# Kernel tuning notes

Measured on AMD Instinct MI355X. Metric: run time of the kernel, lower is better.

## Reference

```python
import jax, jax.numpy as jnp
import numpy as np

# static config (Phi-3-like with GQA)
B, S, H, HKV, D, BS = 2, 2048, 32, 8, 128, 64
HID = H * D
NB = B * (S // BS)  # total cache blocks
THETA = 10000.0


def rotate_half(x):
    x1, x2 = jnp.split(x, 2, axis=-1)
    return jnp.concatenate([-x2, x1], axis=-1)


def rope_cos_sin(positions):
    # positions: [T] int -> cos/sin [T, D]
    inv_freq = 1.0 / (THETA ** (jnp.arange(0, D, 2, dtype=jnp.float32) / D))
    freqs = positions.astype(jnp.float32)[:, None] * inv_freq[None, :]
    emb = jnp.concatenate([freqs, freqs], axis=-1)
    return jnp.cos(emb), jnp.sin(emb)


def setup_inputs() -> dict:
    key = jax.random.key(0)
    k1, k2, k3 = jax.random.split(key, 3)
    T = B * S
    hidden_states = jax.random.normal(k1, (T, HID), dtype=jnp.float32)
    w_qkv = jax.random.normal(k2, ((H + 2 * HKV) * D, HID), dtype=jnp.float32) * 0.02
    w_o = jax.random.normal(k3, (HID, H * D), dtype=jnp.float32) * 0.02
    k_cache = jnp.zeros((NB, BS, HKV, D), dtype=jnp.float32)
    v_cache = jnp.zeros((NB, BS, HKV, D), dtype=jnp.float32)
    position_ids = jnp.tile(jnp.arange(S, dtype=jnp.int32), B)  # per-token positions (prefill)
    block_offsets = jnp.arange(NB, dtype=jnp.int32).reshape(B, S // BS)
    return dict(hidden_states=hidden_states, w_qkv=w_qkv, w_o=w_o,
                k_cache=k_cache, v_cache=v_cache, position_ids=position_ids,
                block_offsets=block_offsets, window_size=1024)


def reference(hidden_states, w_qkv, w_o, k_cache, v_cache, position_ids, block_offsets, window_size):
    # fused qkv projection + split
    qkv = hidden_states @ w_qkv.T  # [T, (H+2*HKV)*D]
    q, k, v = jnp.split(qkv, [H * D, H * D + HKV * D], axis=-1)
    q = q.reshape(-1, H, D)
    k = k.reshape(-1, HKV, D)
    v = v.reshape(-1, HKV, D)

    # rotary embedding on flattened tokens
    cos, sin = rope_cos_sin(position_ids)  # [T, D]
    cos, sin = cos[:, None, :], sin[:, None, :]
    q = q * cos + rotate_half(q) * sin
    k = k * cos + rotate_half(k) * sin

    # fill paged KV cache: token t of seq b -> block block_offsets[b, t//BS], slot t%BS
    flat_blocks = block_offsets.reshape(-1)  # [NB]
    k_blk = k.reshape(NB, BS, HKV, D)
    v_blk = v.reshape(NB, BS, HKV, D)
    k_cache = k_cache.at[flat_blocks].set(k_blk)
    v_cache = v_cache.at[flat_blocks].set(v_blk)

    # paged attention: gather per-sequence K/V through the block table
    k_seq = k_cache[block_offsets].reshape(B, S, HKV, D)
    v_seq = v_cache[block_offsets].reshape(B, S, HKV, D)

    G = H // HKV  # query heads per kv head (GQA)
    qh = q.reshape(B, S, HKV, G, D)
    scale = 1.0 / jnp.sqrt(jnp.float32(D))
    scores = jnp.einsum('bshgd,bthd->bhgst', qh, k_seq) * scale  # [B,HKV,G,S,S]

    # causal + sliding-window mask: j <= i and i - j < window_size
    i = jnp.arange(S)[:, None]
    j = jnp.arange(S)[None, :]
    mask = (j <= i) & ((i - j) < window_size)  # [S,S]
    scores = jnp.where(mask[None, None, None], scores, jnp.finfo(scores.dtype).min)
    probs = jax.nn.softmax(scores, axis=-1)

    out = jnp.einsum('bhgst,bthd->bshgd', probs, v_seq)  # [B,S,HKV,G,D]
    out = out.reshape(B * S, H * D)
    return out @ w_o.T  # [T, HID]
```

## Files before the change

kernel.cpp:

```cpp
#include <hip/hip_runtime.h>
#include <hip/hip_bf16.h>
#include <stdint.h>

typedef unsigned short u16;
typedef __attribute__((ext_vector_type(8))) short short8;
typedef __attribute__((ext_vector_type(8))) unsigned short u16x8;
typedef __attribute__((ext_vector_type(4))) float f32x4;
typedef __attribute__((ext_vector_type(16))) float f32x16;

#define B_    2
#define S_    2048
#define H_    32
#define HKV_  8
#define D_    128
#define HID_  4096
#define QKVW_ 6144

__device__ __forceinline__ u16 f2bf(float f){
  uint32_t b = __builtin_bit_cast(uint32_t, f);
  b += 0x7FFFu + ((b >> 16) & 1u);
  return (u16)(b >> 16);
}
__device__ __forceinline__ float bf2f(u16 h){
  uint32_t b = ((uint32_t)h) << 16;
  return __builtin_bit_cast(float, b);
}
__device__ __forceinline__ u16 bfc(float f){
  __hip_bfloat16 h = __float2bfloat16(f);
  return __builtin_bit_cast(u16, h);
}
__device__ __forceinline__ uint32_t cvtpk(float a, float b){
  uint32_t r;
  asm("v_cvt_pk_bf16_f32 %0, %1, %2" : "=v"(r) : "v"(a), "v"(b));
  return r;
}
__device__ __forceinline__ void pl32swap(uint32_t &a, uint32_t &b){
  asm volatile("v_permlane32_swap_b32 %0, %1" : "+v"(a), "+v"(b));
}

__device__ __forceinline__ void gload16(const u16* g, u16* l){
  __builtin_amdgcn_global_load_lds((const __attribute__((address_space(1))) void*)g,
                                   (__attribute__((address_space(3))) void*)l, 16, 0, 0);
}

__global__ void cvt_kernel(const float* __restrict__ src, u16* __restrict__ dst, int n4){
  int i = blockIdx.x * blockDim.x + threadIdx.x;
  int stride = gridDim.x * blockDim.x;
  for (; i < n4; i += stride){
    float4 v = reinterpret_cast<const float4*>(src)[i];
    union { u16 u[4]; unsigned long long ll; } o;
    o.u[0] = f2bf(v.x); o.u[1] = f2bf(v.y); o.u[2] = f2bf(v.z); o.u[3] = f2bf(v.w);
    reinterpret_cast<unsigned long long*>(dst)[i] = o.ll;
  }
}

__global__ void rope_table_kernel(float2* __restrict__ tab){
  int idx = blockIdx.x * blockDim.x + threadIdx.x;
  if (idx >= S_ * 64) return;
  int pos = idx >> 6, p = idx & 63;
  float inv = powf(10000.0f, -(float)p / 64.0f);
  float ang = (float)pos * inv;
  tab[idx] = make_float2(cosf(ang), sinf(ang));
}

__global__ void rope_k_kernel(u16* __restrict__ qkv, const int* __restrict__ pos_ids,
                              const float2* __restrict__ tab){
  int t = blockIdx.x;
  int pos = pos_ids[t];
  const float2* tb = tab + pos * 64;
  u16* row = qkv + (size_t)t * QKVW_ + HID_;
  for (int it = threadIdx.x; it < HKV_ * 64; it += 256){
    int hh = it >> 6, p = it & 63;
    int base = hh * D_;
    float x1 = bf2f(row[base + p]);
    float x2 = bf2f(row[base + 64 + p]);
    float2 cs = tb[p];
    row[base + p]      = f2bf(x1 * cs.x - x2 * cs.y);
    row[base + 64 + p] = f2bf(x2 * cs.x + x1 * cs.y);
  }
}

#define MFMA_(a, b, c)   __builtin_amdgcn_mfma_f32_16x16x32_bf16((a), (b), (c), 0, 0, 0)
#define MFMA32_(a, b, c) __builtin_amdgcn_mfma_f32_32x32x16_bf16((a), (b), (c), 0, 0, 0)

__global__ __launch_bounds__(256) void gemm128(const u16* __restrict__ A, const u16* __restrict__ B,
                                               u16* __restrict__ C, int M, int N, int K){
  __shared__ u16 As[128*64];
  __shared__ u16 Bs[128*64];
  const int tid  = threadIdx.x;
  const int wave = tid >> 6, lane = tid & 63;
  const int hi = lane >> 4, lo = lane & 15;
  const int bn = blockIdx.x, bm = blockIdx.y;
  const int wm = (wave >> 1) * 64, wn = (wave & 1) * 64;
  f32x4 acc[4][4] = {};

  const u16* ap[4]; const u16* bp[4];
  u16* lA[4]; u16* lB[4];
  #pragma unroll
  for (int p = 0; p < 4; p++){
    int e   = p*2048 + wave*512 + lane*8;
    int row = e >> 6;
    int cs  = ((e >> 3) & 7) ^ (row & 7);
    ap[p] = A + (size_t)(bm*128 + row) * K + cs*8;
    bp[p] = B + (size_t)(bn*128 + row) * K + cs*8;
    lA[p] = &As[p*2048 + wave*512];
    lB[p] = &Bs[p*2048 + wave*512];
  }
  const int sw = lo & 7;
  const int nk = K >> 6;
  for (int t = 0; t < nk; t++){
    #pragma unroll
    for (int p = 0; p < 4; p++){
      gload16(ap[p], lA[p]);
      gload16(bp[p], lB[p]);
      ap[p] += 64; bp[p] += 64;
    }
    __syncthreads();
    #pragma unroll
    for (int kk = 0; kk < 2; kk++){
      short8 af[4], bf[4];
      int sz = ((kk*4 + hi) ^ sw) * 8;
      #pragma unroll
      for (int mt = 0; mt < 4; mt++) af[mt] = *(const short8*)&As[(wm + mt*16 + lo)*64 + sz];
      #pragma unroll
      for (int nt = 0; nt < 4; nt++) bf[nt] = *(const short8*)&Bs[(wn + nt*16 + lo)*64 + sz];
      #pragma unroll
      for (int mt = 0; mt < 4; mt++)
        #pragma unroll
        for (int nt = 0; nt < 4; nt++)
          acc[mt][nt] = MFMA_(af[mt], bf[nt], acc[mt][nt]);
    }
    __syncthreads();
  }
  #pragma unroll
  for (int mt = 0; mt < 4; mt++){
    int row = bm*128 + wm + mt*16 + 4*hi;
    #pragma unroll
    for (int nt = 0; nt < 4; nt++){
      int col = bn*128 + wn + nt*16 + lo;
      #pragma unroll
      for (int r = 0; r < 4; r++)
        C[(size_t)(row + r)*N + col] = f2bf(acc[mt][nt][r]);
    }
  }
}

__global__ __launch_bounds__(512, 2) void gemm256(const u16* __restrict__ A, const u16* __restrict__ B,
                                                  float* __restrict__ C, int M, int N, int K, int nbn){
  __shared__ u16 As[2][16384];
  __shared__ u16 Bs[2][16384];
  const int tid = threadIdx.x;
  const int wave = tid >> 6, lane = tid & 63, lo = lane & 15, hi = lane >> 4;
  const int wr = wave >> 2, wc = wave & 3;
  const int sw = lo & 7;

  const int nwg = gridDim.x, bid = blockIdx.x, cpx = nwg >> 3;
  const int wg = (bid & 7) * cpx + (bid >> 3);
  const int bm = wg / nbn, bn = wg - bm * nbn;

  f32x4 acc[8][4] = {};

  const int pr0 = tid >> 3;
  const int sc0 = (tid & 7) ^ (pr0 & 7);
  const u16* aS0 = A + ((size_t)(bm*256 + pr0      ))*K + sc0*8;
  const u16* aS1 = A + ((size_t)(bm*256 + pr0 + 128))*K + sc0*8;
  const u16* aS2 = A + ((size_t)(bm*256 + pr0 + 64 ))*K + sc0*8;
  const u16* aS3 = A + ((size_t)(bm*256 + pr0 + 192))*K + sc0*8;
  const u16* bS0 = B + ((size_t)(bn*256 + pr0      ))*K + sc0*8;
  const u16* bS1 = B + ((size_t)(bn*256 + pr0 + 64 ))*K + sc0*8;
  const u16* bS2 = B + ((size_t)(bn*256 + pr0 + 128))*K + sc0*8;
  const u16* bS3 = B + ((size_t)(bn*256 + pr0 + 192))*K + sc0*8;
  const int dOfs = tid * 8;

  gload16(bS0, &Bs[0][dOfs]);        gload16(bS1, &Bs[0][4096 + dOfs]);
  gload16(bS2, &Bs[0][8192 + dOfs]); gload16(bS3, &Bs[0][12288 + dOfs]);
  gload16(aS0, &As[0][dOfs]);        gload16(aS1, &As[0][4096 + dOfs]);
  gload16(aS2, &As[0][8192 + dOfs]); gload16(aS3, &As[0][12288 + dOfs]);
  asm volatile("s_waitcnt vmcnt(0)" ::: "memory");
  __builtin_amdgcn_s_barrier();

  const int nk = K >> 6;
  for (int t = 0; t < nk; ++t){
    const int cur = t & 1, nxt = cur ^ 1;
    const u16* Ac = &As[cur][0];
    const u16* Bc = &Bs[cur][0];
    u16* An = &As[nxt][0];
    u16* Bn = &Bs[nxt][0];
    const size_t ko = (size_t)(t + 1) * 64;
    const bool more = (t + 1 < nk);
    short8 avr[4], bvr[8];

    #define RD_A(q) \
      _Pragma("unroll") for (int mt = 0; mt < 2; mt++) \
        _Pragma("unroll") for (int kk = 0; kk < 2; kk++){ \
          int ra = wr*128 + (q)*32 + mt*16 + lo; \
          int fo = ((ra & 63) << 6) + ((ra & 64) ? 8192 : 0) + ((ra & 128) ? 4096 : 0) \
                 + ((((kk << 2) + hi) ^ sw) << 3); \
          avr[mt*2 + kk] = *(const short8*)&Ac[fo]; \
        }
    #define DO_MFMA(q) \
      __builtin_amdgcn_s_setprio(1); \
      _Pragma("unroll") for (int mt = 0; mt < 2; mt++) \
        _Pragma("unroll") for (int nt = 0; nt < 4; nt++) \
          _Pragma("unroll") for (int kk = 0; kk < 2; kk++) \
            acc[(q)*2 + mt][nt] = MFMA_(avr[mt*2 + kk], bvr[nt*2 + kk], acc[(q)*2 + mt][nt]); \
      __builtin_amdgcn_s_setprio(0);

    #pragma unroll
    for (int nt = 0; nt < 4; nt++)
      #pragma unroll
      for (int kk = 0; kk < 2; kk++){
        int rb = wc*64 + nt*16 + lo;
        int fo = (rb << 6) + ((((kk << 2) + hi) ^ sw) << 3);
        bvr[nt*2 + kk] = *(const short8*)&Bc[fo];
      }
    RD_A(0)
    if (more){ gload16(bS0 + ko, Bn + dOfs); gload16(bS1 + ko, Bn + 4096 + dOfs); }
    __builtin_amdgcn_s_barrier();
    DO_MFMA(0)
    __builtin_amdgcn_s_barrier();

    RD_A(1)
    if (more){
      gload16(bS2 + ko, Bn + 8192 + dOfs); gload16(bS3 + ko, Bn + 12288 + dOfs);
      asm volatile("s_waitcnt vmcnt(4)" ::: "memory");
    } else {
      asm volatile("s_waitcnt vmcnt(0)" ::: "memory");
    }
    __builtin_amdgcn_sched_barrier(0);
    __builtin_amdgcn_s_barrier();
    DO_MFMA(1)
    __builtin_amdgcn_s_barrier();

    RD_A(2)
    if (more){ gload16(aS0 + ko, An + dOfs); gload16(aS1 + ko, An + 4096 + dOfs); }
    __builtin_amdgcn_s_barrier();
    DO_MFMA(2)
    __builtin_amdgcn_s_barrier();

    RD_A(3)
    if (more){ gload16(aS2 + ko, An + 8192 + dOfs); gload16(aS3 + ko, An + 12288 + dOfs); }
    asm volatile("s_waitcnt vmcnt(2)" ::: "memory");
    __builtin_amdgcn_sched_barrier(0);
    __builtin_amdgcn_s_barrier();
    DO_MFMA(3)
    __builtin_amdgcn_s_barrier();
    #undef RD_A
    #undef DO_MFMA
  }

  #pragma unroll
  for (int mtg = 0; mtg < 8; mtg++){
    int row = bm*256 + wr*128 + mtg*16 + 4*hi;
    #pragma unroll
    for (int nt = 0; nt < 4; nt++){
      int col = bn*256 + wc*64 + nt*16 + lo;
      #pragma unroll
      for (int r = 0; r < 4; r++)
        C[(size_t)(row + r)*N + col] = acc[mtg][nt][r];
    }
  }
}

__global__ __launch_bounds__(256, 2) void attn_kernel(const u16* __restrict__ qkv, u16* __restrict__ out,
                                                      const int* __restrict__ winp,
                                                      const int* __restrict__ pos_ids,
                                                      const float2* __restrict__ tab){
  const int id = blockIdx.x;
  const int hkv = id & 7;
  const int qtr = (id >> 3) & 15;
  const int gb  = id >> 7;
  const int qt  = (qtr + 3*gb) & 15;
  const int g = gb & 3, b = gb >> 2;
  const int h = hkv*4 + g;
  const int q0 = qt * 128;
  const int tid = threadIdx.x, wave = tid >> 6, lane = tid & 63;
  const int ql = lane & 31, hl = lane >> 5;
  const int win = winp[0];

  __shared__ u16 Ks[2][64*128];
  __shared__ u16 VT[2][128*64];

  const int qw = q0 + wave*32;
  short8 qf[8];
  {
    const u16* qp = qkv + (size_t)(b*S_ + qw + ql)*QKVW_ + h*D_ + hl*8;
    #pragma unroll
    for (int c = 0; c < 8; c++) qf[c] = *(const short8*)(qp + c*16);
    const float QS = 0.08838834764831845f * 1.4426950408889634f;
    int pos = pos_ids[b*S_ + qw + ql];
    const float2* tb = tab + pos*64 + hl*8;
    #pragma unroll
    for (int c = 0; c < 4; c++)
      #pragma unroll
      for (int i = 0; i < 8; i++){
        float2 cs = tb[c*16 + i];
        float x1 = bf2f((u16)qf[c][i]), x2 = bf2f((u16)qf[c+4][i]);
        qf[c][i]   = (short)bfc((x1*cs.x - x2*cs.y) * QS);
        qf[c+4][i] = (short)bfc((x2*cs.x + x1*cs.y) * QS);
      }
  }

  f32x16 acc[4] = {};
  float m_r = -3.0e38f, l_r = 0.0f;

  int js = q0 - (win - 1); if (js < 0) js = 0; js &= ~63;
  const int nt = (q0 + 128 - js) >> 6;

  const u16* Kg = qkv + (size_t)HID_ + hkv*D_;
  const u16* Vg = qkv + (size_t)HID_ + HKV_*D_ + hkv*D_;
  const int jp = tid & 31, d0 = (tid >> 5) * 16;

  const u16* ksrc[4];
  #pragma unroll
  for (int p = 0; p < 4; p++){
    int e = p*256 + tid;
    int row = e >> 4;
    int ss = (e & 15) ^ (row & 15);
    ksrc[p] = Kg + (size_t)(b*S_ + js + row)*QKVW_ + ss*8;
  }
  const u16* vsrc = Vg + (size_t)(b*S_ + js + 2*jp)*QKVW_ + d0;

  u16x8 vr0, vr1, vr2, vr3;
  {
    #pragma unroll
    for (int p = 0; p < 4; p++) gload16(ksrc[p], &Ks[0][p*2048 + wave*512]);
    vr0 = *(const u16x8*)(vsrc);
    vr1 = *(const u16x8*)(vsrc + 8);
    vr2 = *(const u16x8*)(vsrc + QKVW_);
    vr3 = *(const u16x8*)(vsrc + QKVW_ + 8);
    uint32_t* VT32 = (uint32_t*)&VT[0][0];
    #pragma unroll
    for (int i = 0; i < 8; i++){
      int da = d0 + i, db = d0 + 8 + i;
      VT32[da*32 + (jp ^ ((da & 7) << 2))] = (uint32_t)vr0[i] | ((uint32_t)vr2[i] << 16);
      VT32[db*32 + (jp ^ ((db & 7) << 2))] = (uint32_t)vr1[i] | ((uint32_t)vr3[i] << 16);
    }
  }
  __syncthreads();

  for (int t = 0; t < nt; t++){
    const int jc = js + t*64;
    const int cur = t & 1, nxt = cur ^ 1;
    const bool more = (t + 1 < nt);
    if (more){
      const size_t adv = (size_t)(t+1) * 64 * QKVW_;
      #pragma unroll
      for (int p = 0; p < 4; p++) gload16(ksrc[p] + adv, &Ks[nxt][p*2048 + wave*512]);
      const u16* vp = vsrc + adv;
      vr0 = *(const u16x8*)(vp);
      vr1 = *(const u16x8*)(vp + 8);
      vr2 = *(const u16x8*)(vp + QKVW_);
      vr3 = *(const u16x8*)(vp + QKVW_ + 8);
    }
    if (jc <= qw + 31 && jc + 63 >= qw - win + 1){
      f32x16 s0 = {}, s1 = {};
      const int sl = ql & 15;
      __builtin_amdgcn_s_setprio(1);
      #pragma unroll
      for (int c = 0; c < 8; c++){
        int so = (((c*2 + hl) ^ sl) * 8);
        short8 k0 = *(const short8*)&Ks[cur][ql*128 + so];
        short8 k1 = *(const short8*)&Ks[cur][(32 + ql)*128 + so];
        s0 = MFMA32_(k0, qf[c], s0);
        s1 = MFMA32_(k1, qf[c], s1);
      }
      __builtin_amdgcn_s_setprio(0);
      const int qa = qw + ql;
      const bool fullv = (jc + 63 <= qw) && (jc >= qw + 32 - win);
      if (!fullv){
        #pragma unroll
        for (int r = 0; r < 16; r++){
          int j0 = jc + (r&3) + 8*(r>>2) + 4*hl;
          if (j0 > qa || qa - j0 >= win) s0[r] = -3.0e38f;
          int j1 = j0 + 32;
          if (j1 > qa || qa - j1 >= win) s1[r] = -3.0e38f;
        }
      }
      float mx = s0[0];
      #pragma unroll
      for (int r = 1; r < 16; r++) mx = fmaxf(mx, s0[r]);
      #pragma unroll
      for (int r = 0; r < 16; r++) mx = fmaxf(mx, s1[r]);
      mx = fmaxf(mx, __shfl_xor(mx, 32));
      if (__any(mx > m_r + 8.0f)){
        float mn = fmaxf(m_r, mx);
        float al = exp2f(m_r - mn);
        m_r = mn; l_r *= al;
        #pragma unroll
        for (int r = 0; r < 16; r++){
          float a = __shfl(al, (r&3) + 8*(r>>2) + 4*hl);
          acc[0][r] *= a; acc[1][r] *= a; acc[2][r] *= a; acc[3][r] *= a;
        }
      }
      float ps = 0.f;
      if (fullv){
        #pragma unroll
        for (int r = 0; r < 16; r++){
          s0[r] = exp2f(s0[r] - m_r); s1[r] = exp2f(s1[r] - m_r);
          ps += s0[r] + s1[r];
        }
      } else {
        #pragma unroll
        for (int r = 0; r < 16; r++){
          s0[r] = s0[r] > -1e37f ? exp2f(s0[r] - m_r) : 0.f;
          s1[r] = s1[r] > -1e37f ? exp2f(s1[r] - m_r) : 0.f;
          ps += s0[r] + s1[r];
        }
      }
      ps += __shfl_xor(ps, 32);
      l_r += ps;
      short8 pa[4];
      #define MKFRAG(dst, P, o) { \
        uint32_t x1 = cvtpk(P[o+0], P[o+1]), x2 = cvtpk(P[o+2], P[o+3]); \
        uint32_t y1 = cvtpk(P[o+4], P[o+5]), y2 = cvtpk(P[o+6], P[o+7]); \
        pl32swap(x1, y1); pl32swap(x2, y2); \
        union { uint32_t w[4]; short8 v; } u_; \
        u_.w[0] = x1; u_.w[1] = x2; u_.w[2] = y1; u_.w[3] = y2; \
        dst = u_.v; }
      MKFRAG(pa[0], s0, 0)
      MKFRAG(pa[1], s0, 8)
      MKFRAG(pa[2], s1, 0)
      MKFRAG(pa[3], s1, 8)
      #undef MKFRAG
      __builtin_amdgcn_s_setprio(1);
      #pragma unroll
      for (int dt = 0; dt < 4; dt++){
        const int dr = dt*32 + ql;
        const u16* vb = &VT[cur][dr*64];
        const int sb = dr & 7;
        #pragma unroll
        for (int ks = 0; ks < 4; ks++){
          short8 vf = *(const short8*)&vb[(((ks*2 + hl) ^ sb) * 8)];
          acc[dt] = MFMA32_(pa[ks], vf, acc[dt]);
        }
      }
      __builtin_amdgcn_s_setprio(0);
    }
    if (more){
      uint32_t* VT32 = (uint32_t*)&VT[nxt][0];
      #pragma unroll
      for (int i = 0; i < 8; i++){
        int da = d0 + i, db = d0 + 8 + i;
        VT32[da*32 + (jp ^ ((da & 7) << 2))] = (uint32_t)vr0[i] | ((uint32_t)vr2[i] << 16);
        VT32[db*32 + (jp ^ ((db & 7) << 2))] = (uint32_t)vr1[i] | ((uint32_t)vr3[i] << 16);
      }
      __syncthreads();
    }
  }
  #pragma unroll
  for (int r = 0; r < 16; r++){
    int qrow = (r&3) + 8*(r>>2) + 4*hl;
    float lr = __shfl(l_r, qrow);
    float invl = 1.0f / lr;
    size_t ro = (size_t)(b*S_ + qw + qrow)*HID_ + h*D_ + ql;
    out[ro     ] = f2bf(acc[0][r] * invl);
    out[ro + 32] = f2bf(acc[1][r] * invl);
    out[ro + 64] = f2bf(acc[2][r] * invl);
    out[ro + 96] = f2bf(acc[3][r] * invl);
  }
}

extern "C" void kernel_launch(void* const* d_in, const int* in_sizes, int n_in,
                              void* d_out, int out_size, void* d_ws, size_t ws_size,
                              hipStream_t stream) {
  const float* hs   = (const float*)d_in[0];
  const float* wqkv = (const float*)d_in[1];
  const float* wo   = (const float*)d_in[2];
  const int* pos  = (const int*)d_in[5];
  const int* winp = (const int*)d_in[7];
  float* out = (float*)d_out;

  u16* hsb = (u16*)d_ws;
  u16* wqb = hsb + (size_t)HID_*HID_;
  u16* wob = wqb + (size_t)QKVW_*HID_;
  u16* qkv = wob + (size_t)HID_*HID_;
  u16* att = qkv + (size_t)(B_*S_)*QKVW_;
  float2* tab = (float2*)(att + (size_t)(B_*S_)*HID_);

  cvt_kernel<<<2048, 256, 0, stream>>>(hs,   hsb, HID_*HID_/4);
  cvt_kernel<<<2048, 256, 0, stream>>>(wqkv, wqb, QKVW_*HID_/4);
  cvt_kernel<<<2048, 256, 0, stream>>>(wo,   wob, HID_*HID_/4);
  rope_table_kernel<<<(S_*64 + 255)/256, 256, 0, stream>>>(tab);
  gemm128<<<dim3(QKVW_/128, (B_*S_)/128), 256, 0, stream>>>(hsb, wqb, qkv, B_*S_, QKVW_, HID_);
  rope_k_kernel<<<B_*S_, 256, 0, stream>>>(qkv, pos, tab);
  attn_kernel<<<1024, 256, 0, stream>>>(qkv, att, winp, pos, tab);
  gemm256<<<(B_*S_/256)*(HID_/256), 512, 0, stream>>>(att, wob, out, B_*S_, HID_, HID_, HID_/256);
}
```

Baseline: 524.7 us.

## Replace QKV projection GEMM with templated 256x192 double-buffered pipelined GEMM

```diff
diff --git a/kernel.cpp b/kernel.cpp
--- a/kernel.cpp
+++ b/kernel.cpp
@@ -83,72 +83,13 @@
 #define MFMA_(a, b, c)   __builtin_amdgcn_mfma_f32_16x16x32_bf16((a), (b), (c), 0, 0, 0)
 #define MFMA32_(a, b, c) __builtin_amdgcn_mfma_f32_32x32x16_bf16((a), (b), (c), 0, 0, 0)
 
-__global__ __launch_bounds__(256) void gemm128(const u16* __restrict__ A, const u16* __restrict__ B,
-                                               u16* __restrict__ C, int M, int N, int K){
-  __shared__ u16 As[128*64];
-  __shared__ u16 Bs[128*64];
-  const int tid  = threadIdx.x;
-  const int wave = tid >> 6, lane = tid & 63;
-  const int hi = lane >> 4, lo = lane & 15;
-  const int bn = blockIdx.x, bm = blockIdx.y;
-  const int wm = (wave >> 1) * 64, wn = (wave & 1) * 64;
-  f32x4 acc[4][4] = {};
-
-  const u16* ap[4]; const u16* bp[4];
-  u16* lA[4]; u16* lB[4];
-  #pragma unroll
-  for (int p = 0; p < 4; p++){
-    int e   = p*2048 + wave*512 + lane*8;
-    int row = e >> 6;
-    int cs  = ((e >> 3) & 7) ^ (row & 7);
-    ap[p] = A + (size_t)(bm*128 + row) * K + cs*8;
-    bp[p] = B + (size_t)(bn*128 + row) * K + cs*8;
-    lA[p] = &As[p*2048 + wave*512];
-    lB[p] = &Bs[p*2048 + wave*512];
-  }
-  const int sw = lo & 7;
-  const int nk = K >> 6;
-  for (int t = 0; t < nk; t++){
-    #pragma unroll
-    for (int p = 0; p < 4; p++){
-      gload16(ap[p], lA[p]);
-      gload16(bp[p], lB[p]);
-      ap[p] += 64; bp[p] += 64;
-    }
-    __syncthreads();
-    #pragma unroll
-    for (int kk = 0; kk < 2; kk++){
-      short8 af[4], bf[4];
-      int sz = ((kk*4 + hi) ^ sw) * 8;
-      #pragma unroll
-      for (int mt = 0; mt < 4; mt++) af[mt] = *(const short8*)&As[(wm + mt*16 + lo)*64 + sz];
-      #pragma unroll
-      for (int nt = 0; nt < 4; nt++) bf[nt] = *(const short8*)&Bs[(wn + nt*16 + lo)*64 + sz];
-      #pragma unroll
-      for (int mt = 0; mt < 4; mt++)
-        #pragma unroll
-        for (int nt = 0; nt < 4; nt++)
-          acc[mt][nt] = MFMA_(af[mt], bf[nt], acc[mt][nt]);
-    }
-    __syncthreads();
-  }
-  #pragma unroll
-  for (int mt = 0; mt < 4; mt++){
-    int row = bm*128 + wm + mt*16 + 4*hi;
-    #pragma unroll
-    for (int nt = 0; nt < 4; nt++){
-      int col = bn*128 + wn + nt*16 + lo;
-      #pragma unroll
-      for (int r = 0; r < 4; r++)
-        C[(size_t)(row + r)*N + col] = f2bf(acc[mt][nt][r]);
-    }
-  }
-}
-
-__global__ __launch_bounds__(512, 2) void gemm256(const u16* __restrict__ A, const u16* __restrict__ B,
-                                                  float* __restrict__ C, int M, int N, int K, int nbn){
+template<int BN, int CF>
+__global__ __launch_bounds__(512, 2) void gemmN(const u16* __restrict__ A, const u16* __restrict__ B,
+                                                void* __restrict__ Cv, int M, int N, int K, int nbn){
+  constexpr int NBP = BN / 64;
+  constexpr int WN  = BN / 4;
   __shared__ u16 As[2][16384];
-  __shared__ u16 Bs[2][16384];
+  __shared__ u16 Bs[2][BN*64];
   const int tid = threadIdx.x;
   const int wave = tid >> 6, lane = tid & 63, lo = lane & 15, hi = lane >> 4;
   const int wr = wave >> 2, wc = wave & 3;
@@ -158,7 +99,7 @@
   const int wg = (bid & 7) * cpx + (bid >> 3);
   const int bm = wg / nbn, bn = wg - bm * nbn;
 
-  f32x4 acc[8][4] = {};
+  f32x4 acc[8][NBP] = {};
 
   const int pr0 = tid >> 3;
   const int sc0 = (tid & 7) ^ (pr0 & 7);
@@ -166,14 +107,14 @@
   const u16* aS1 = A + ((size_t)(bm*256 + pr0 + 128))*K + sc0*8;
   const u16* aS2 = A + ((size_t)(bm*256 + pr0 + 64 ))*K + sc0*8;
   const u16* aS3 = A + ((size_t)(bm*256 + pr0 + 192))*K + sc0*8;
-  const u16* bS0 = B + ((size_t)(bn*256 + pr0      ))*K + sc0*8;
-  const u16* bS1 = B + ((size_t)(bn*256 + pr0 + 64 ))*K + sc0*8;
-  const u16* bS2 = B + ((size_t)(bn*256 + pr0 + 128))*K + sc0*8;
-  const u16* bS3 = B + ((size_t)(bn*256 + pr0 + 192))*K + sc0*8;
+  const u16* bS[NBP];
+  #pragma unroll
+  for (int p = 0; p < NBP; p++)
+    bS[p] = B + ((size_t)(bn*BN + pr0 + p*64))*K + sc0*8;
   const int dOfs = tid * 8;
 
-  gload16(bS0, &Bs[0][dOfs]);        gload16(bS1, &Bs[0][4096 + dOfs]);
-  gload16(bS2, &Bs[0][8192 + dOfs]); gload16(bS3, &Bs[0][12288 + dOfs]);
+  #pragma unroll
+  for (int p = 0; p < NBP; p++) gload16(bS[p], &Bs[0][p*4096 + dOfs]);
   gload16(aS0, &As[0][dOfs]);        gload16(aS1, &As[0][4096 + dOfs]);
   gload16(aS2, &As[0][8192 + dOfs]); gload16(aS3, &As[0][12288 + dOfs]);
   asm volatile("s_waitcnt vmcnt(0)" ::: "memory");
@@ -188,7 +129,7 @@
     u16* Bn = &Bs[nxt][0];
     const size_t ko = (size_t)(t + 1) * 64;
     const bool more = (t + 1 < nk);
-    short8 avr[4], bvr[8];
+    short8 avr[4], bvr[2*NBP];
 
     #define RD_A(q) \
       _Pragma("unroll") for (int mt = 0; mt < 2; mt++) \
@@ -201,28 +142,32 @@
     #define DO_MFMA(q) \
       __builtin_amdgcn_s_setprio(1); \
       _Pragma("unroll") for (int mt = 0; mt < 2; mt++) \
-        _Pragma("unroll") for (int nt = 0; nt < 4; nt++) \
+        _Pragma("unroll") for (int nt = 0; nt < NBP; nt++) \
           _Pragma("unroll") for (int kk = 0; kk < 2; kk++) \
             acc[(q)*2 + mt][nt] = MFMA_(avr[mt*2 + kk], bvr[nt*2 + kk], acc[(q)*2 + mt][nt]); \
       __builtin_amdgcn_s_setprio(0);
 
     #pragma unroll
-    for (int nt = 0; nt < 4; nt++)
+    for (int nt = 0; nt < NBP; nt++)
       #pragma unroll
       for (int kk = 0; kk < 2; kk++){
-        int rb = wc*64 + nt*16 + lo;
+        int rb = wc*WN + nt*16 + lo;
         int fo = (rb << 6) + ((((kk << 2) + hi) ^ sw) << 3);
         bvr[nt*2 + kk] = *(const short8*)&Bc[fo];
       }
     RD_A(0)
-    if (more){ gload16(bS0 + ko, Bn + dOfs); gload16(bS1 + ko, Bn + 4096 + dOfs); }
+    if (more){ gload16(bS[0] + ko, Bn + dOfs); gload16(bS[1] + ko, Bn + 4096 + dOfs); }
     __builtin_amdgcn_s_barrier();
     DO_MFMA(0)
     __builtin_amdgcn_s_barrier();
 
     RD_A(1)
     if (more){
-      gload16(bS2 + ko, Bn + 8192 + dOfs); gload16(bS3 + ko, Bn + 12288 + dOfs);
+      if constexpr (NBP == 4){
+        gload16(bS[2] + ko, Bn + 8192 + dOfs); gload16(bS[3] + ko, Bn + 12288 + dOfs);
+      } else {
+        gload16(bS[2] + ko, Bn + 8192 + dOfs); gload16(aS0 + ko, An + dOfs);
+      }
       asm volatile("s_waitcnt vmcnt(4)" ::: "memory");
     } else {
       asm volatile("s_waitcnt vmcnt(0)" ::: "memory");
@@ -233,13 +178,25 @@
     __builtin_amdgcn_s_barrier();
 
     RD_A(2)
-    if (more){ gload16(aS0 + ko, An + dOfs); gload16(aS1 + ko, An + 4096 + dOfs); }
+    if (more){
+      if constexpr (NBP == 4){
+        gload16(aS0 + ko, An + dOfs); gload16(aS1 + ko, An + 4096 + dOfs);
+      } else {
+        gload16(aS1 + ko, An + 4096 + dOfs); gload16(aS2 + ko, An + 8192 + dOfs);
+      }
+    }
     __builtin_amdgcn_s_barrier();
     DO_MFMA(2)
     __builtin_amdgcn_s_barrier();
 
     RD_A(3)
-    if (more){ gload16(aS2 + ko, An + 8192 + dOfs); gload16(aS3 + ko, An + 12288 + dOfs); }
+    if (more){
+      if constexpr (NBP == 4){
+        gload16(aS2 + ko, An + 8192 + dOfs); gload16(aS3 + ko, An + 12288 + dOfs);
+      } else {
+        gload16(aS3 + ko, An + 12288 + dOfs);
+      }
+    }
     asm volatile("s_waitcnt vmcnt(2)" ::: "memory");
     __builtin_amdgcn_sched_barrier(0);
     __builtin_amdgcn_s_barrier();
@@ -253,11 +210,13 @@
   for (int mtg = 0; mtg < 8; mtg++){
     int row = bm*256 + wr*128 + mtg*16 + 4*hi;
     #pragma unroll
-    for (int nt = 0; nt < 4; nt++){
-      int col = bn*256 + wc*64 + nt*16 + lo;
-      #pragma unroll
-      for (int r = 0; r < 4; r++)
-        C[(size_t)(row + r)*N + col] = acc[mtg][nt][r];
+    for (int nt = 0; nt < NBP; nt++){
+      int col = bn*BN + wc*WN + nt*16 + lo;
+      #pragma unroll
+      for (int r = 0; r < 4; r++){
+        if (CF == 0) ((u16*)Cv)[(size_t)(row + r)*N + col] = f2bf(acc[mtg][nt][r]);
+        else         ((float*)Cv)[(size_t)(row + r)*N + col] = acc[mtg][nt][r];
+      }
     }
   }
 }
@@ -482,8 +441,8 @@
   cvt_kernel<<<2048, 256, 0, stream>>>(wqkv, wqb, QKVW_*HID_/4);
   cvt_kernel<<<2048, 256, 0, stream>>>(wo,   wob, HID_*HID_/4);
   rope_table_kernel<<<(S_*64 + 255)/256, 256, 0, stream>>>(tab);
-  gemm128<<<dim3(QKVW_/128, (B_*S_)/128), 256, 0, stream>>>(hsb, wqb, qkv, B_*S_, QKVW_, HID_);
+  gemmN<192,0><<<(B_*S_/256)*(QKVW_/192), 512, 0, stream>>>(hsb, wqb, (void*)qkv, B_*S_, QKVW_, HID_, QKVW_/192);
   rope_k_kernel<<<B_*S_, 256, 0, stream>>>(qkv, pos, tab);
   attn_kernel<<<1024, 256, 0, stream>>>(qkv, att, winp, pos, tab);
-  gemm256<<<(B_*S_/256)*(HID_/256), 512, 0, stream>>>(att, wob, out, B_*S_, HID_, HID_, HID_/256);
-}
+  gemmN<256,1><<<(B_*S_/256)*(HID_/256), 512, 0, stream>>>(att, wob, (void*)out, B_*S_, HID_, HID_, HID_/256);
+}
```

Result: slower. 543.0 us (+3.5%).
